# Performance work log

Measured on AMD Instinct MI355X. Metric: run time of the kernel, lower is better.

The kernel has to match this reference:

```python
import jax, jax.numpy as jnp
import numpy as np

K_REGIONS = 1024   # number of FPS centroids (regions)
RADIUS = 0.4       # ball-query radius
NSAMPLE = 64       # samples per group
EPS = 1e-5         # BatchNorm eps


def setup_inputs() -> dict:
    key = jax.random.key(0)
    ks = jax.random.split(key, 8)
    B, N = 16, 4096
    pc = jax.random.normal(ks[0], (B, 3, N), jnp.float32)

    def conv_w(k, o, i):
        return jax.random.normal(k, (o, i), jnp.float32) * (1.0 / np.sqrt(i))

    return {
        "point_cloud": pc,
        "w1": conv_w(ks[1], 64, 3),  "b1": jnp.zeros(64),  "gamma1": jnp.ones(64),  "beta1": jnp.zeros(64),
        "w2": conv_w(ks[2], 64, 64), "b2": jnp.zeros(64),  "gamma2": jnp.ones(64),  "beta2": jnp.zeros(64),
        "w3": conv_w(ks[3], 128, 64),"b3": jnp.zeros(128), "gamma3": jnp.ones(128), "beta3": jnp.zeros(128),
    }


def farthest_point_sample(xyz, k):
    # xyz: (B, N, 3) -> indices (B, k). Inherently sequential; scan over k steps.
    B, N, _ = xyz.shape

    def step(carry, _):
        min_d, farthest = carry                      # (B,N), (B,)
        centroid = jnp.take_along_axis(xyz, farthest[:, None, None], axis=1)  # (B,1,3)
        d = jnp.sum((xyz - centroid) ** 2, axis=-1)  # (B,N)
        min_d = jnp.minimum(min_d, d)
        nxt = jnp.argmax(min_d, axis=-1).astype(jnp.int32)
        return (min_d, nxt), farthest

    init = (jnp.full((B, N), 1e10, jnp.float32), jnp.zeros((B,), jnp.int32))
    _, idxs = jax.lax.scan(step, init, None, length=k)
    return idxs.T  # (B, k)


def ball_query(xyz, centroids, radius, n):
    # xyz (B,N,3), centroids (B,K,3) -> group indices (B,K,n)
    B, N, _ = xyz.shape
    # squared distances via ||a||^2 + ||b||^2 - 2 a.b
    c2 = jnp.sum(centroids ** 2, -1)[:, :, None]          # (B,K,1)
    x2 = jnp.sum(xyz ** 2, -1)[:, None, :]                # (B,1,N)
    sqd = c2 + x2 - 2.0 * jnp.einsum('bkc,bnc->bkn', centroids, xyz)  # (B,K,N)
    idx = jnp.where(sqd <= radius * radius, jnp.arange(N, dtype=jnp.int32)[None, None, :], N)
    idx = jnp.sort(idx, axis=-1)[:, :, :n]                # first n in-radius (padded with N)
    first = idx[:, :, :1]                                 # centroid itself is always in-radius
    return jnp.where(idx == N, first, idx)


def _mlp_layer(x, w, b, g, beta):
    # 1x1 Conv2d + BatchNorm2d (training-mode batch stats) + ReLU; x: (B,C,n,K)
    y = jnp.einsum('oc,bcnk->bonk', w, x) + b[None, :, None, None]
    m = y.mean(axis=(0, 2, 3), keepdims=True)
    v = y.var(axis=(0, 2, 3), keepdims=True)
    y = (y - m) * jax.lax.rsqrt(v + EPS) * g[None, :, None, None] + beta[None, :, None, None]
    return jax.nn.relu(y)


def reference(point_cloud, w1, b1, gamma1, beta1, w2, b2, gamma2, beta2, w3, b3, gamma3, beta3):
    xyz = point_cloud.transpose(0, 2, 1)                  # (B,N,3)
    B = xyz.shape[0]
    fps_idx = farthest_point_sample(xyz, K_REGIONS)       # (B,K)
    centroids = xyz[jnp.arange(B)[:, None], fps_idx]      # (B,K,3)
    gidx = ball_query(xyz, centroids, RADIUS, NSAMPLE)    # (B,K,n)
    grouped = xyz[jnp.arange(B)[:, None, None], gidx]     # (B,K,n,3)
    grouped = grouped - centroids[:, :, None, :]          # relative coords
    x = grouped.transpose(0, 3, 2, 1)                     # (B,3,n,K)  == permute(0,3,2,1)
    x = _mlp_layer(x, w1, b1, gamma1, beta1)
    x = _mlp_layer(x, w2, b2, gamma2, beta2)
    x = _mlp_layer(x, w3, b3, gamma3, beta3)
    feats = jnp.max(x, axis=2)                            # max over neighbor dim n -> (B,128,K)
    return centroids.transpose(0, 2, 1), feats            # (B,3,K), (B,128,K)
```

## Files before the change

### kernel.cpp

```cpp
#include <hip/hip_runtime.h>
#include <stdint.h>

#define NPTS 4096
#define KREG 1024
#define NS   64
#define NB   16
#define PTOT (NB*KREG*NS)
#define NWAVE (PTOT/64)
#define GATH_BLOCKS 256

typedef float v2f __attribute__((ext_vector_type(2)));
typedef __attribute__((ext_vector_type(8))) short bf16x8;
typedef __attribute__((ext_vector_type(4))) float f32x4;

__device__ __forceinline__ unsigned short f2bf(float v) {
    unsigned u = __float_as_uint(v);
    u += 0x7FFFu + ((u >> 16) & 1u);
    return (unsigned short)(u >> 16);
}

#define DPPF(v, ctrl) __int_as_float(__builtin_amdgcn_mov_dpp( \
        __float_as_int(v), ctrl, 0xF, 0xF, true))

__global__ __launch_bounds__(256) void fps_kernel(
    const float* __restrict__ pc, float* __restrict__ outC)
{
#pragma clang fp contract(off)
    __shared__ float4 pcL[NPTS];
    __shared__ alignas(16) unsigned long long wpart[2][4];

    const int b = blockIdx.x;
    const int t = threadIdx.x;
    const int wv = t >> 6;
    const int lane = t & 63;
    const float* px = pc + (size_t)b * 3 * NPTS;

    v2f lx[8], ly[8], lz[8], md[8];
    {
        const float4* px4 = (const float4*)(px + t * 16);
        const float4* py4 = (const float4*)(px + NPTS + t * 16);
        const float4* pz4 = (const float4*)(px + 2 * NPTS + t * 16);
        #pragma unroll
        for (int q = 0; q < 4; ++q) {
            float4 xx = px4[q], yy = py4[q], zz = pz4[q];
            lx[2*q]   = (v2f){xx.x, xx.y};  lx[2*q+1] = (v2f){xx.z, xx.w};
            ly[2*q]   = (v2f){yy.x, yy.y};  ly[2*q+1] = (v2f){yy.z, yy.w};
            lz[2*q]   = (v2f){zz.x, zz.y};  lz[2*q+1] = (v2f){zz.z, zz.w};
            md[2*q]   = (v2f){1e10f, 1e10f};
            md[2*q+1] = (v2f){1e10f, 1e10f};
            pcL[(4*q + 0) * 256 + t] = make_float4(xx.x, yy.x, zz.x, 0.f);
            pcL[(4*q + 1) * 256 + t] = make_float4(xx.y, yy.y, zz.y, 0.f);
            pcL[(4*q + 2) * 256 + t] = make_float4(xx.z, yy.z, zz.z, 0.f);
            pcL[(4*q + 3) * 256 + t] = make_float4(xx.w, yy.w, zz.w, 0.f);
        }
    }
    __syncthreads();
    float4 cc = pcL[0];

    for (int it = 0; it < KREG; ++it) {
        if (t == 0) {
            pcL[it].w        = cc.x;
            pcL[1024 + it].w = cc.y;
            pcL[2048 + it].w = cc.z;
        }
        const v2f cx2 = (v2f){cc.x, cc.x};
        const v2f cy2 = (v2f){cc.y, cc.y};
        const v2f cz2 = (v2f){cc.z, cc.z};
        float mbest = -1.0f;
        int jbest = 0;
        #pragma unroll
        for (int q = 0; q < 8; ++q) {
            v2f dx = lx[q] - cx2;
            v2f dy = ly[q] - cy2;
            v2f dz = lz[q] - cz2;
            v2f d  = (dx * dx + dy * dy) + dz * dz;
            v2f m;
            m.x = fminf(md[q].x, d.x);
            m.y = fminf(md[q].y, d.y);
            md[q] = m;
            if (m.x > mbest) { mbest = m.x; jbest = 2 * q; }
            if (m.y > mbest) { mbest = m.y; jbest = 2 * q + 1; }
        }
        float r = mbest;
        r = fmaxf(r, DPPF(r, 0xB1));
        r = fmaxf(r, DPPF(r, 0x4E));
        r = fmaxf(r, DPPF(r, 0x141));
        r = fmaxf(r, DPPF(r, 0x140));
        r = fmaxf(r, DPPF(r, 0x142));
        r = fmaxf(r, DPPF(r, 0x143));
        float mxw = __int_as_float(
            __builtin_amdgcn_readlane(__float_as_int(r), 63));
        unsigned long long ball = __ballot(mbest == mxw);
        int L = __ffsll((long long)ball) - 1;
        int jw = __builtin_amdgcn_readlane(jbest, L);
        unsigned pw = ((unsigned)(wv * 64 + L) << 4) + (unsigned)jw;
        unsigned long long key =
            ((unsigned long long)__float_as_uint(mxw) << 32) |
            (unsigned long long)(0xFFFFFFFFu - pw);
        if (lane == 0) wpart[it & 1][wv] = key;
        __syncthreads();
        const unsigned long long* wp = &wpart[it & 1][0];
        ulonglong2 k01 = *(const ulonglong2*)&wp[0];
        ulonglong2 k23 = *(const ulonglong2*)&wp[2];
        unsigned long long ka = (k01.x > k01.y) ? k01.x : k01.y;
        unsigned long long kb = (k23.x > k23.y) ? k23.x : k23.y;
        unsigned long long kk = (ka > kb) ? ka : kb;
        int f = (int)(0xFFFFFFFFu - (unsigned)kk);
        cc = pcL[(f & 15) * 256 + (f >> 4)];
    }
    __syncthreads();
    for (int i = t; i < KREG; i += 256) {
        outC[(size_t)b * 3 * KREG + i]            = pcL[i].w;
        outC[(size_t)b * 3 * KREG + KREG + i]     = pcL[1024 + i].w;
        outC[(size_t)b * 3 * KREG + 2 * KREG + i] = pcL[2048 + i].w;
    }
}

__global__ __launch_bounds__(256) void ballquery_kernel(
    const float* __restrict__ pc, const float* __restrict__ outC,
    int* __restrict__ gidx)
{
    int gw = blockIdx.x * 4 + (threadIdx.x >> 6);
    int lane = threadIdx.x & 63;
    int b = gw >> 10;
    int k = gw & (KREG - 1);
    const float* px = pc + (size_t)b * 3 * NPTS;

    float cx = outC[(size_t)b * 3 * KREG + k];
    float cy = outC[(size_t)b * 3 * KREG + KREG + k];
    float cz = outC[(size_t)b * 3 * KREG + 2 * KREG + k];
    float c2 = __fadd_rn(__fadd_rn(__fmul_rn(cx, cx), __fmul_rn(cy, cy)),
                         __fmul_rn(cz, cz));
    const float r2 = 0.16f;
    int base = gw * NS;
    int cnt = 0;
    int firstidx = -1;

    for (int nb = 0; nb < NPTS / 64; ++nb) {
        int n = nb * 64 + lane;
        float x = px[n], y = px[NPTS + n], z = px[2 * NPTS + n];
        float x2 = __fadd_rn(__fadd_rn(__fmul_rn(x, x), __fmul_rn(y, y)),
                             __fmul_rn(z, z));
        float dt = __fadd_rn(__fadd_rn(__fmul_rn(cx, x), __fmul_rn(cy, y)),
                             __fmul_rn(cz, z));
        float sqd = __fsub_rn(__fadd_rn(c2, x2), __fmul_rn(2.0f, dt));
        bool pred = (sqd <= r2);
        unsigned long long mask = __ballot(pred);
        if (firstidx < 0 && mask) firstidx = nb * 64 + __ffsll((long long)mask) - 1;
        int pos = cnt + __popcll(mask & ((1ull << lane) - 1ull));
        if (pred && pos < NS) gidx[base + pos] = n;
        cnt += __popcll(mask);
        if (cnt >= NS) break;
    }
    if (lane >= cnt) gidx[base + lane] = firstidx;
}

__global__ __launch_bounds__(256) void gather_kernel(
    const float* __restrict__ pc, const float* __restrict__ outC,
    const int* __restrict__ gidx, float* __restrict__ X0,
    float* __restrict__ mpart)
{
    float a[9] = {0, 0, 0, 0, 0, 0, 0, 0, 0};
    for (int p = blockIdx.x * 256 + threadIdx.x; p < PTOT; p += GATH_BLOCKS * 256) {
        int bk = p >> 6;
        int b = bk >> 10;
        int k = bk & (KREG - 1);
        int idx = gidx[p];
        const float* px = pc + (size_t)b * 3 * NPTS;
        float x = px[idx]            - outC[(size_t)b * 3 * KREG + k];
        float y = px[NPTS + idx]     - outC[(size_t)b * 3 * KREG + KREG + k];
        float z = px[2 * NPTS + idx] - outC[(size_t)b * 3 * KREG + 2 * KREG + k];
        X0[p] = x; X0[PTOT + p] = y; X0[2 * PTOT + p] = z;
        a[0] += x;     a[1] += y;     a[2] += z;
        a[3] += x * x; a[4] += y * y; a[5] += z * z;
        a[6] += x * y; a[7] += x * z; a[8] += y * z;
    }
    __shared__ float red[4][9];
    int wv = threadIdx.x >> 6;
    #pragma unroll
    for (int q = 0; q < 9; ++q) {
        float v = a[q];
        #pragma unroll
        for (int s = 32; s > 0; s >>= 1) v += __shfl_xor(v, s, 64);
        if ((threadIdx.x & 63) == 0) red[wv][q] = v;
    }
    __syncthreads();
    if (threadIdx.x < 9) {
        mpart[blockIdx.x * 9 + threadIdx.x] =
            red[0][threadIdx.x] + red[1][threadIdx.x] +
            red[2][threadIdx.x] + red[3][threadIdx.x];
    }
}

__global__ void bn1_finalize(
    const float* __restrict__ mpart, const float* __restrict__ w1,
    const float* __restrict__ b1, const float* __restrict__ g1,
    const float* __restrict__ be1, float* __restrict__ sc1,
    float* __restrict__ sh1)
{
    __shared__ double M[9];
    int t = threadIdx.x;
    if (t < 9) {
        double s = 0;
        for (int i = 0; i < GATH_BLOCKS; ++i) s += (double)mpart[i * 9 + t];
        M[t] = s / (double)PTOT;
    }
    __syncthreads();
    if (t < 64) {
        double mux = M[0], muy = M[1], muz = M[2];
        double xx = M[3], yy = M[4], zz = M[5], xy = M[6], xz = M[7], yz = M[8];
        double wx = w1[t * 3], wy = w1[t * 3 + 1], wz = w1[t * 3 + 2], bb = b1[t];
        double wmu = wx * mux + wy * muy + wz * muz;
        double mean = wmu + bb;
        double ey2 = wx * wx * xx + wy * wy * yy + wz * wz * zz
                   + 2.0 * (wx * wy * xy + wx * wz * xz + wy * wz * yz)
                   + 2.0 * bb * wmu + bb * bb;
        double var = ey2 - mean * mean;
        double scale = (double)g1[t] / sqrt(var + 1e-5);
        sc1[t] = (float)scale;
        sh1[t] = (float)((double)be1[t] - mean * scale);
    }
}

__global__ __launch_bounds__(256) void prep_kernel(
    const float* __restrict__ w2, const float* __restrict__ w3,
    unsigned short* __restrict__ w2h, unsigned short* __restrict__ w3h)
{
    int t = blockIdx.x * 256 + threadIdx.x;
    if (t < 4096) w2h[t] = f2bf(w2[t]);
    if (t < 8192) w3h[t] = f2bf(w3[t]);
}

#define MFMA_HI2(acc, ah0, bh0, ah1, bh1)                                      \
    acc = __builtin_amdgcn_mfma_f32_16x16x32_bf16(ah0, bh0, acc, 0, 0, 0);     \
    acc = __builtin_amdgcn_mfma_f32_16x16x32_bf16(ah1, bh1, acc, 0, 0, 0);

__global__ __launch_bounds__(256) void conv12_stats_kernel(
    const float* __restrict__ X0,
    const float* __restrict__ w1, const float* __restrict__ b1,
    const float* __restrict__ sc1, const float* __restrict__ sh1,
    const unsigned short* __restrict__ w2h, const float* __restrict__ b2,
    float* __restrict__ sum2, float* __restrict__ sq2)
{
    __shared__ alignas(16) unsigned short X1h[128 * 64];
    const int t = threadIdx.x;
    const int pos = t & 127;
    const int half = __builtin_amdgcn_readfirstlane(t >> 7);
    const int p = blockIdx.x * 128 + pos;

    float x = X0[p], y = X0[PTOT + p], z = X0[2 * PTOT + p];
    const int sw = (pos & 7) << 4;
    #pragma unroll
    for (int o2 = 0; o2 < 16; ++o2) {
        int oo = half * 32 + o2 * 2;
        float v0 = b1[oo];
        v0 = fmaf(w1[oo * 3 + 2], z, v0);
        v0 = fmaf(w1[oo * 3 + 1], y, v0);
        v0 = fmaf(w1[oo * 3 + 0], x, v0);
        v0 = fmaxf(fmaf(v0, sc1[oo], sh1[oo]), 0.f);
        float v1 = b1[oo + 1];
        v1 = fmaf(w1[oo * 3 + 5], z, v1);
        v1 = fmaf(w1[oo * 3 + 4], y, v1);
        v1 = fmaf(w1[oo * 3 + 3], x, v1);
        v1 = fmaxf(fmaf(v1, sc1[oo + 1], sh1[oo + 1]), 0.f);
        unsigned short h0 = f2bf(v0), h1 = f2bf(v1);
        int boff = pos * 128 + ((oo * 2) ^ sw);
        *(unsigned*)((char*)X1h + boff) = (unsigned)h0 | ((unsigned)h1 << 16);
    }
    __syncthreads();

    const int wv2 = __builtin_amdgcn_readfirstlane(t >> 6);
    const int lcol = t & 15;
    const int lk = (t & 63) >> 4;

    bf16x8 ah[2];
    #pragma unroll
    for (int kh = 0; kh < 2; ++kh) {
        int idx = (wv2 * 16 + lcol) * 64 + kh * 32 + lk * 8;
        ah[kh] = *(const bf16x8*)(w2h + idx);
    }
    f32x4 b2v = *(const f32x4*)&b2[wv2 * 16 + lk * 4];

    float ssm[2][4] = {{0}}, ssq[2][4] = {{0}};
    #pragma unroll
    for (int nt = 0; nt < 8; ++nt) {
        const int g = nt >> 2;
        int prow = nt * 16 + lcol;
        int rb = prow * 128;
        int psw = (prow & 7) << 4;
        bf16x8 bh[2];
        #pragma unroll
        for (int kh = 0; kh < 2; ++kh) {
            int off = rb + ((kh * 64 + lk * 16) ^ psw);
            bh[kh] = *(const bf16x8*)((const char*)X1h + off);
        }
        f32x4 acc = {0.f, 0.f, 0.f, 0.f};
        MFMA_HI2(acc, ah[0], bh[0], ah[1], bh[1])
        #pragma unroll
        for (int r = 0; r < 4; ++r) {
            float v = acc[r] + b2v[r];
            ssm[g][r] += v;
            ssq[g][r] = fmaf(v, v, ssq[g][r]);
        }
    }
    #pragma unroll
    for (int g = 0; g < 2; ++g) {
        #pragma unroll
        for (int r = 0; r < 4; ++r) {
            float s = ssm[g][r];
            s += DPPF(s, 0xB1);  s += DPPF(s, 0x4E);
            s += DPPF(s, 0x141); s += DPPF(s, 0x140);
            float q = ssq[g][r];
            q += DPPF(q, 0xB1);  q += DPPF(q, 0x4E);
            q += DPPF(q, 0x141); q += DPPF(q, 0x140);
            if (lcol == 0) {
                int o = wv2 * 16 + lk * 4 + r;
                size_t gw = (size_t)(blockIdx.x * 2 + g);
                sum2[(size_t)o * NWAVE + gw] = s;
                sq2[(size_t)o * NWAVE + gw] = q;
            }
        }
    }
}

__global__ __launch_bounds__(256) void bn_finalize_kernel(
    const float* __restrict__ sumb, const float* __restrict__ sqb,
    const float* __restrict__ g, const float* __restrict__ be,
    float* __restrict__ sc, float* __restrict__ sh)
{
    int o = blockIdx.x, t = threadIdx.x;
    double s = 0, q = 0;
    for (int i = t; i < NWAVE; i += 256) {
        s += (double)sumb[(size_t)o * NWAVE + i];
        q += (double)sqb[(size_t)o * NWAVE + i];
    }
    #pragma unroll
    for (int m = 32; m > 0; m >>= 1) {
        s += __shfl_xor(s, m, 64);
        q += __shfl_xor(q, m, 64);
    }
    __shared__ double rs[4], rq[4];
    if ((t & 63) == 0) { rs[t >> 6] = s; rq[t >> 6] = q; }
    __syncthreads();
    if (t == 0) {
        s = rs[0] + rs[1] + rs[2] + rs[3];
        q = rq[0] + rq[1] + rq[2] + rq[3];
        double mean = s / (double)PTOT;
        double var = q / (double)PTOT - mean * mean;
        double scale = (double)g[o] / sqrt(var + 1e-5);
        sc[o] = (float)scale;
        sh[o] = (float)((double)be[o] - mean * scale);
    }
}

__global__ __launch_bounds__(256) void conv123_kernel(
    const float* __restrict__ X0,
    const float* __restrict__ w1, const float* __restrict__ b1,
    const float* __restrict__ sc1, const float* __restrict__ sh1,
    const unsigned short* __restrict__ w2h, const float* __restrict__ b2,
    const float* __restrict__ sc2, const float* __restrict__ sh2,
    const unsigned short* __restrict__ w3h, const float* __restrict__ b3,
    float* __restrict__ y3max, float* __restrict__ y3min,
    float* __restrict__ sum3, float* __restrict__ sq3)
{
    __shared__ alignas(16) unsigned short X1h[128 * 64];
    __shared__ alignas(16) unsigned short X2h[128 * 64];
    __shared__ alignas(16) float b3L[128];

    const int t = threadIdx.x;
    const int pos = t & 127;
    const int half = __builtin_amdgcn_readfirstlane(t >> 7);
    const int p = blockIdx.x * 128 + pos;
    if (t < 128) b3L[t] = b3[t];

    float x = X0[p], y = X0[PTOT + p], z = X0[2 * PTOT + p];
    const int sw = (pos & 7) << 4;
    #pragma unroll
    for (int o2 = 0; o2 < 16; ++o2) {
        int oo = half * 32 + o2 * 2;
        float v0 = b1[oo];
        v0 = fmaf(w1[oo * 3 + 2], z, v0);
        v0 = fmaf(w1[oo * 3 + 1], y, v0);
        v0 = fmaf(w1[oo * 3 + 0], x, v0);
        v0 = fmaxf(fmaf(v0, sc1[oo], sh1[oo]), 0.f);
        float v1 = b1[oo + 1];
        v1 = fmaf(w1[oo * 3 + 5], z, v1);
        v1 = fmaf(w1[oo * 3 + 4], y, v1);
        v1 = fmaf(w1[oo * 3 + 3], x, v1);
        v1 = fmaxf(fmaf(v1, sc1[oo + 1], sh1[oo + 1]), 0.f);
        unsigned short h0 = f2bf(v0), h1 = f2bf(v1);
        int boff = pos * 128 + ((oo * 2) ^ sw);
        *(unsigned*)((char*)X1h + boff) = (unsigned)h0 | ((unsigned)h1 << 16);
    }
    __syncthreads();

    const int wv2 = __builtin_amdgcn_readfirstlane(t >> 6);
    const int lcol = t & 15;
    const int lk = (t & 63) >> 4;

    {
        bf16x8 ah[2];
        #pragma unroll
        for (int kh = 0; kh < 2; ++kh) {
            int idx = (wv2 * 16 + lcol) * 64 + kh * 32 + lk * 8;
            ah[kh] = *(const bf16x8*)(w2h + idx);
        }
        f32x4 b2v = *(const f32x4*)&b2[wv2 * 16 + lk * 4];
        f32x4 sc2v = *(const f32x4*)&sc2[wv2 * 16 + lk * 4];
        f32x4 sh2v = *(const f32x4*)&sh2[wv2 * 16 + lk * 4];
        const int ch0 = wv2 * 16 + lk * 4;

        #pragma unroll
        for (int nt = 0; nt < 8; ++nt) {
            int prow = nt * 16 + lcol;
            int rb = prow * 128;
            int psw = (prow & 7) << 4;
            bf16x8 bh[2];
            #pragma unroll
            for (int kh = 0; kh < 2; ++kh) {
                int off = rb + ((kh * 64 + lk * 16) ^ psw);
                bh[kh] = *(const bf16x8*)((const char*)X1h + off);
            }
            f32x4 acc = {0.f, 0.f, 0.f, 0.f};
            MFMA_HI2(acc, ah[0], bh[0], ah[1], bh[1])
            unsigned short hh[4];
            #pragma unroll
            for (int r = 0; r < 4; ++r) {
                float v = acc[r] + b2v[r];
                float x2 = fmaxf(fmaf(v, sc2v[r], sh2v[r]), 0.f);
                hh[r] = f2bf(x2);
            }
            int b0 = prow * 128 + ((ch0 * 2) ^ psw);
            *(unsigned*)((char*)X2h + b0)     = (unsigned)hh[0] | ((unsigned)hh[1] << 16);
            *(unsigned*)((char*)X2h + b0 + 4) = (unsigned)hh[2] | ((unsigned)hh[3] << 16);
        }
    }
    __syncthreads();

    bf16x8 ah3[2][2];
    f32x4 bias[2];
    #pragma unroll
    for (int mt = 0; mt < 2; ++mt) {
        #pragma unroll
        for (int kh = 0; kh < 2; ++kh) {
            int m = (wv2 * 2 + mt) * 16 + lcol;
            int idx = m * 64 + kh * 32 + lk * 8;
            ah3[mt][kh] = *(const bf16x8*)(w3h + idx);
        }
        bias[mt] = *(const f32x4*)&b3L[(wv2 * 2 + mt) * 16 + lk * 4];
    }

    float smx[2][2][4], smn[2][2][4], ssm[2][2][4], ssq[2][2][4];
    #pragma unroll
    for (int g = 0; g < 2; ++g)
        #pragma unroll
        for (int mt = 0; mt < 2; ++mt)
            #pragma unroll
            for (int r = 0; r < 4; ++r) {
                smx[g][mt][r] = -1e30f; smn[g][mt][r] = 1e30f;
                ssm[g][mt][r] = 0.f;    ssq[g][mt][r] = 0.f;
            }

    #pragma unroll
    for (int nt = 0; nt < 8; ++nt) {
        const int g = nt >> 2;
        int prow = nt * 16 + lcol;
        int rb = prow * 128;
        int psw = (prow & 7) << 4;
        bf16x8 bh[2];
        #pragma unroll
        for (int kh = 0; kh < 2; ++kh) {
            int off = rb + ((kh * 64 + lk * 16) ^ psw);
            bh[kh] = *(const bf16x8*)((const char*)X2h + off);
        }
        #pragma unroll
        for (int mt = 0; mt < 2; ++mt) {
            f32x4 acc = {0.f, 0.f, 0.f, 0.f};
            MFMA_HI2(acc, ah3[mt][0], bh[0], ah3[mt][1], bh[1])
            #pragma unroll
            for (int r = 0; r < 4; ++r) {
                float v = acc[r] + bias[mt][r];
                smx[g][mt][r] = fmaxf(smx[g][mt][r], v);
                smn[g][mt][r] = fminf(smn[g][mt][r], v);
                ssm[g][mt][r] += v;
                ssq[g][mt][r] = fmaf(v, v, ssq[g][mt][r]);
            }
        }
    }

    #pragma unroll
    for (int g = 0; g < 2; ++g) {
        #pragma unroll
        for (int mt = 0; mt < 2; ++mt) {
            #pragma unroll
            for (int r = 0; r < 4; ++r) {
                float a = smx[g][mt][r];
                a = fmaxf(a, DPPF(a, 0xB1));  a = fmaxf(a, DPPF(a, 0x4E));
                a = fmaxf(a, DPPF(a, 0x141)); a = fmaxf(a, DPPF(a, 0x140));
                float c = smn[g][mt][r];
                c = fminf(c, DPPF(c, 0xB1));  c = fminf(c, DPPF(c, 0x4E));
                c = fminf(c, DPPF(c, 0x141)); c = fminf(c, DPPF(c, 0x140));
                float s = ssm[g][mt][r];
                s += DPPF(s, 0xB1);  s += DPPF(s, 0x4E);
                s += DPPF(s, 0x141); s += DPPF(s, 0x140);
                float q = ssq[g][mt][r];
                q += DPPF(q, 0xB1);  q += DPPF(q, 0x4E);
                q += DPPF(q, 0x141); q += DPPF(q, 0x140);
                if (lcol == 0) {
                    int o = (wv2 * 2 + mt) * 16 + lk * 4 + r;
                    size_t gw = (size_t)(blockIdx.x * 2 + g);
                    y3max[gw * 128 + o] = a;
                    y3min[gw * 128 + o] = c;
                    sum3[(size_t)o * NWAVE + gw] = s;
                    sq3[(size_t)o * NWAVE + gw] = q;
                }
            }
        }
    }
}

__global__ __launch_bounds__(256) void feats_kernel(
    const float* __restrict__ y3max, const float* __restrict__ y3min,
    const float* __restrict__ sc3, const float* __restrict__ sh3,
    float* __restrict__ feats)
{
    __shared__ float tile[64][129];
    int blk = blockIdx.x;
    int b = blk >> 4, kt = blk & 15;
    int t = threadIdx.x;
    size_t bk0 = (size_t)(b * KREG + kt * 64);
    #pragma unroll
    for (int i = 0; i < 32; ++i) {
        int idx = i * 256 + t;
        int o = idx & 127, kk = idx >> 7;
        float a = sc3[o];
        float v = (a >= 0.f) ? y3max[(bk0 + kk) * 128 + o]
                             : y3min[(bk0 + kk) * 128 + o];
        tile[kk][o] = fmaxf(fmaf(v, a, sh3[o]), 0.0f);
    }
    __syncthreads();
    #pragma unroll
    for (int i = 0; i < 32; ++i) {
        int idx = i * 256 + t;
        int kk = idx & 63, o = idx >> 6;
        feats[(size_t)b * 128 * KREG + (size_t)o * KREG + kt * 64 + kk] = tile[kk][o];
    }
}

extern "C" void kernel_launch(void* const* d_in, const int* in_sizes, int n_in,
                              void* d_out, int out_size, void* d_ws, size_t ws_size,
                              hipStream_t stream)
{
    const float* pc  = (const float*)d_in[0];
    const float* w1  = (const float*)d_in[1];
    const float* b1  = (const float*)d_in[2];
    const float* g1  = (const float*)d_in[3];
    const float* be1 = (const float*)d_in[4];
    const float* w2  = (const float*)d_in[5];
    const float* b2  = (const float*)d_in[6];
    const float* g2  = (const float*)d_in[7];
    const float* be2 = (const float*)d_in[8];
    const float* w3  = (const float*)d_in[9];
    const float* b3  = (const float*)d_in[10];
    const float* g3  = (const float*)d_in[11];
    const float* be3 = (const float*)d_in[12];

    float* outC  = (float*)d_out;
    float* feats = (float*)d_out + NB * 3 * KREG;

    const size_t MB = 1024 * 1024;
    char* ws = (char*)d_ws;
    int*   gidx  = (int*)ws;
    float* X0    = (float*)(ws + 4 * MB);
    float* mpart = (float*)(ws + 16 * MB);
    float* sc1   = (float*)(ws + 16 * MB + 16 * 1024);
    float* sh1   = (float*)(ws + 16 * MB + 17 * 1024);
    float* sc2   = (float*)(ws + 16 * MB + 18 * 1024);
    float* sh2   = (float*)(ws + 16 * MB + 19 * 1024);
    float* sc3   = (float*)(ws + 16 * MB + 20 * 1024);
    float* sh3   = (float*)(ws + 16 * MB + 21 * 1024);
    unsigned short* w2h = (unsigned short*)(ws + 16 * MB + 32 * 1024);
    unsigned short* w3h = (unsigned short*)(ws + 16 * MB + 64 * 1024);
    float* sum2  = (float*)(ws + 17 * MB);
    float* sq2   = (float*)(ws + 21 * MB);
    float* sum3  = (float*)(ws + 25 * MB);
    float* sq3   = (float*)(ws + 33 * MB);
    float* y3max = (float*)(ws + 41 * MB);
    float* y3min = (float*)(ws + 49 * MB);

    fps_kernel<<<NB, 256, 0, stream>>>(pc, outC);
    ballquery_kernel<<<(NB * KREG) / 4, 256, 0, stream>>>(pc, outC, gidx);
    gather_kernel<<<GATH_BLOCKS, 256, 0, stream>>>(pc, outC, gidx, X0, mpart);
    bn1_finalize<<<1, 64, 0, stream>>>(mpart, w1, b1, g1, be1, sc1, sh1);
    prep_kernel<<<32, 256, 0, stream>>>(w2, w3, w2h, w3h);
    conv12_stats_kernel<<<PTOT / 128, 256, 0, stream>>>(
        X0, w1, b1, sc1, sh1, w2h, b2, sum2, sq2);
    bn_finalize_kernel<<<64, 256, 0, stream>>>(sum2, sq2, g2, be2, sc2, sh2);
    conv123_kernel<<<PTOT / 128, 256, 0, stream>>>(
        X0, w1, b1, sc1, sh1, w2h, b2, sc2, sh2, w3h, b3,
        y3max, y3min, sum3, sq3);
    bn_finalize_kernel<<<128, 256, 0, stream>>>(sum3, sq3, g3, be3, sc3, sh3);
    feats_kernel<<<NB * (KREG / 64), 256, 0, stream>>>(y3max, y3min, sc3, sh3, feats);
}
```

Measured before the change: 859.8 us.

## Tree-reduce FPS per-lane argmax and batch four centroids per ball-query wave

In the FPS loop, the serial running argmax over the 16 per-lane distances becomes a pairwise tree reduction, shortening the dependency chain on the sequential critical path. The ball-query kernel now handles four centroids per wave, so each loaded point and its squared norm serve four distance tests, and the grid shrinks by four. This cuts point-cloud loads and loop overhead per centroid, but a wave only exits once all four centroids have 64 neighbours, so divergent early exits can add wasted iterations.

```diff
diff --git a/kernel.cpp b/kernel.cpp
--- a/kernel.cpp
+++ b/kernel.cpp
@@ -66,21 +66,44 @@
         const v2f cx2 = (v2f){cc.x, cc.x};
         const v2f cy2 = (v2f){cc.y, cc.y};
         const v2f cz2 = (v2f){cc.z, cc.z};
-        float mbest = -1.0f;
-        int jbest = 0;
+        float m[16];
         #pragma unroll
         for (int q = 0; q < 8; ++q) {
             v2f dx = lx[q] - cx2;
             v2f dy = ly[q] - cy2;
             v2f dz = lz[q] - cz2;
             v2f d  = (dx * dx + dy * dy) + dz * dz;
-            v2f m;
-            m.x = fminf(md[q].x, d.x);
-            m.y = fminf(md[q].y, d.y);
-            md[q] = m;
-            if (m.x > mbest) { mbest = m.x; jbest = 2 * q; }
-            if (m.y > mbest) { mbest = m.y; jbest = 2 * q + 1; }
-        }
+            v2f mm;
+            mm.x = fminf(md[q].x, d.x);
+            mm.y = fminf(md[q].y, d.y);
+            md[q] = mm;
+            m[2*q] = mm.x; m[2*q+1] = mm.y;
+        }
+        float v8[8]; int j8[8];
+        #pragma unroll
+        for (int k = 0; k < 8; ++k) {
+            bool g = m[2*k+1] > m[2*k];
+            v8[k] = g ? m[2*k+1] : m[2*k];
+            j8[k] = g ? 2*k+1 : 2*k;
+        }
+        float v4[4]; int j4[4];
+        #pragma unroll
+        for (int k = 0; k < 4; ++k) {
+            bool g = v8[2*k+1] > v8[2*k];
+            v4[k] = g ? v8[2*k+1] : v8[2*k];
+            j4[k] = g ? j8[2*k+1] : j8[2*k];
+        }
+        float vv[2]; int jj[2];
+        #pragma unroll
+        for (int k = 0; k < 2; ++k) {
+            bool g = v4[2*k+1] > v4[2*k];
+            vv[k] = g ? v4[2*k+1] : v4[2*k];
+            jj[k] = g ? j4[2*k+1] : j4[2*k];
+        }
+        bool gf = vv[1] > vv[0];
+        float mbest = gf ? vv[1] : vv[0];
+        int jbest = gf ? jj[1] : jj[0];
+
         float r = mbest;
         r = fmaxf(r, DPPF(r, 0xB1));
         r = fmaxf(r, DPPF(r, 0x4E));
@@ -120,39 +143,53 @@
     const float* __restrict__ pc, const float* __restrict__ outC,
     int* __restrict__ gidx)
 {
-    int gw = blockIdx.x * 4 + (threadIdx.x >> 6);
-    int lane = threadIdx.x & 63;
-    int b = gw >> 10;
-    int k = gw & (KREG - 1);
+    const int wv = threadIdx.x >> 6;
+    const int lane = threadIdx.x & 63;
+    const int gw0 = (blockIdx.x * 4 + wv) * 4;
+    const int b = gw0 >> 10;
+    const int k0 = gw0 & (KREG - 1);
     const float* px = pc + (size_t)b * 3 * NPTS;
 
-    float cx = outC[(size_t)b * 3 * KREG + k];
-    float cy = outC[(size_t)b * 3 * KREG + KREG + k];
-    float cz = outC[(size_t)b * 3 * KREG + 2 * KREG + k];
-    float c2 = __fadd_rn(__fadd_rn(__fmul_rn(cx, cx), __fmul_rn(cy, cy)),
-                         __fmul_rn(cz, cz));
+    float cx[4], cy[4], cz[4], c2[4];
+    int cnt[4] = {0, 0, 0, 0};
+    int firstidx[4] = {-1, -1, -1, -1};
+    #pragma unroll
+    for (int c = 0; c < 4; ++c) {
+        cx[c] = outC[(size_t)b * 3 * KREG + k0 + c];
+        cy[c] = outC[(size_t)b * 3 * KREG + KREG + k0 + c];
+        cz[c] = outC[(size_t)b * 3 * KREG + 2 * KREG + k0 + c];
+        c2[c] = __fadd_rn(__fadd_rn(__fmul_rn(cx[c], cx[c]),
+                                    __fmul_rn(cy[c], cy[c])),
+                          __fmul_rn(cz[c], cz[c]));
+    }
     const float r2 = 0.16f;
-    int base = gw * NS;
-    int cnt = 0;
-    int firstidx = -1;
 
     for (int nb = 0; nb < NPTS / 64; ++nb) {
         int n = nb * 64 + lane;
         float x = px[n], y = px[NPTS + n], z = px[2 * NPTS + n];
         float x2 = __fadd_rn(__fadd_rn(__fmul_rn(x, x), __fmul_rn(y, y)),
                              __fmul_rn(z, z));
-        float dt = __fadd_rn(__fadd_rn(__fmul_rn(cx, x), __fmul_rn(cy, y)),
-                             __fmul_rn(cz, z));
-        float sqd = __fsub_rn(__fadd_rn(c2, x2), __fmul_rn(2.0f, dt));
-        bool pred = (sqd <= r2);
-        unsigned long long mask = __ballot(pred);
-        if (firstidx < 0 && mask) firstidx = nb * 64 + __ffsll((long long)mask) - 1;
-        int pos = cnt + __popcll(mask & ((1ull << lane) - 1ull));
-        if (pred && pos < NS) gidx[base + pos] = n;
-        cnt += __popcll(mask);
-        if (cnt >= NS) break;
-    }
-    if (lane >= cnt) gidx[base + lane] = firstidx;
+        #pragma unroll
+        for (int c = 0; c < 4; ++c) {
+            if (cnt[c] >= NS) continue;
+            float dt = __fadd_rn(__fadd_rn(__fmul_rn(cx[c], x),
+                                           __fmul_rn(cy[c], y)),
+                                 __fmul_rn(cz[c], z));
+            float sqd = __fsub_rn(__fadd_rn(c2[c], x2), __fmul_rn(2.0f, dt));
+            bool pred = (sqd <= r2);
+            unsigned long long mask = __ballot(pred);
+            if (firstidx[c] < 0 && mask)
+                firstidx[c] = nb * 64 + __ffsll((long long)mask) - 1;
+            int pos = cnt[c] + __popcll(mask & ((1ull << lane) - 1ull));
+            if (pred && pos < NS) gidx[(gw0 + c) * NS + pos] = n;
+            cnt[c] += __popcll(mask);
+        }
+        if (cnt[0] >= NS && cnt[1] >= NS && cnt[2] >= NS && cnt[3] >= NS)
+            break;
+    }
+    #pragma unroll
+    for (int c = 0; c < 4; ++c)
+        if (lane >= cnt[c]) gidx[(gw0 + c) * NS + lane] = firstidx[c];
 }
 
 __global__ __launch_bounds__(256) void gather_kernel(
@@ -589,7 +626,7 @@
     float* y3min = (float*)(ws + 49 * MB);
 
     fps_kernel<<<NB, 256, 0, stream>>>(pc, outC);
-    ballquery_kernel<<<(NB * KREG) / 4, 256, 0, stream>>>(pc, outC, gidx);
+    ballquery_kernel<<<(NB * KREG) / 16, 256, 0, stream>>>(pc, outC, gidx);
     gather_kernel<<<GATH_BLOCKS, 256, 0, stream>>>(pc, outC, gidx, X0, mpart);
     bn1_finalize<<<1, 64, 0, stream>>>(mpart, w1, b1, g1, be1, sc1, sh1);
     prep_kernel<<<32, 256, 0, stream>>>(w2, w3, w2h, w3h);
```

Measured after the change: 981.2 us. 14.1% more time.
